# Kernel optimization log

Measured on AMD Instinct MI355X. Metric: run time of the kernel, lower is better.

Reference implementation:

```python
import jax, jax.numpy as jnp
import numpy as np
import math

D_MODEL, NHEAD, FACTOR = 512, 8, 5

def setup_inputs() -> dict:
    key = jax.random.key(0)
    ks = jax.random.split(key, 9)
    B, L = 4, 2048
    s = 0.02
    inp = {"x": jax.random.normal(ks[0], (B, L, D_MODEL), dtype=jnp.float32)}
    names = ["Wq", "bq", "Wk", "bk", "Wv", "bv", "Wo", "bo"]
    for i, n in enumerate(names):
        k = ks[i + 1]
        if n.startswith("W"):
            inp[n] = jax.random.normal(k, (D_MODEL, D_MODEL), dtype=jnp.float32) * s
        else:
            inp[n] = jnp.zeros((D_MODEL,), dtype=jnp.float32)
    return inp

def reference(x, Wq, bq, Wk, bk, Wv, bv, Wo, bo):
    B, L, _ = x.shape
    H = NHEAD
    D = D_MODEL // H
    # projections -> [B, H, L, D]
    def proj(W, b):
        return (x @ W + b).reshape(B, L, H, D).transpose(0, 2, 1, 3)
    Q, K, V = proj(Wq, bq), proj(Wk, bk), proj(Wv, bv)
    U = min(L, int(FACTOR * math.log(L)) if L > 1 else L)
    scores = jnp.einsum("bhqd,bhkd->bhqk", Q, K) / math.sqrt(D)
    # top-U threshold per query row, mask the rest to -inf
    topk_vals, _ = jax.lax.top_k(scores, U)          # [B,H,L,U]
    thr = topk_vals[..., -1:]                         # [B,H,L,1]
    scores = jnp.where(scores < thr, -jnp.inf, scores)
    attn = jax.nn.softmax(scores, axis=-1)           # dropout p=0 (eval)
    ctx = jnp.einsum("bhqk,bhkd->bhqd", attn, V)     # [B,H,L,D]
    ctx = ctx.transpose(0, 2, 1, 3).reshape(B, L, D_MODEL)
    return ctx @ Wo + bo
```

## Files before the change

### kernel.cpp

```cpp
#include <hip/hip_runtime.h>
#include <cstdint>
#include <cstddef>

#define D_MODEL 512
#define NHEAD   8
#define DH      64
#define B_SZ    4
#define L_SEQ   2048
#define U_TOP   38
#define QPB     8
#define KT      128

__device__ __forceinline__ unsigned mapmono(float f) {
    unsigned u = __float_as_uint(f);
    return (u & 0x80000000u) ? ~u : (u | 0x80000000u);
}

template<int MODE>
__global__ __launch_bounds__(256)
void gemm512(const float* __restrict__ A, const float* __restrict__ W,
             const float* __restrict__ bias, float* __restrict__ C)
{
    __shared__ float As[16][68];
    __shared__ float Bs[16][68];
    const int tid  = threadIdx.x;
    const int row0 = blockIdx.x * 64;
    const int col0 = blockIdx.y * 64;
    const int ty = tid >> 4, tx = tid & 15;
    float acc[4][4] = {};

    for (int kt = 0; kt < D_MODEL; kt += 16) {
        {
            const int m = tid >> 2, k = (tid & 3) << 2;
            const float4 a = *reinterpret_cast<const float4*>(
                &A[(size_t)(row0 + m) * D_MODEL + kt + k]);
            As[k + 0][m] = a.x; As[k + 1][m] = a.y;
            As[k + 2][m] = a.z; As[k + 3][m] = a.w;
        }
        {
            const int k = tid >> 4, n = (tid & 15) << 2;
            *reinterpret_cast<float4*>(&Bs[k][n]) =
                *reinterpret_cast<const float4*>(
                    &W[(size_t)(kt + k) * D_MODEL + col0 + n]);
        }
        __syncthreads();
        #pragma unroll
        for (int kk = 0; kk < 16; ++kk) {
            const float4 a4 = *reinterpret_cast<const float4*>(&As[kk][ty << 2]);
            const float4 b4 = *reinterpret_cast<const float4*>(&Bs[kk][tx << 2]);
            const float av[4] = {a4.x, a4.y, a4.z, a4.w};
            const float bv[4] = {b4.x, b4.y, b4.z, b4.w};
            #pragma unroll
            for (int i = 0; i < 4; ++i)
                #pragma unroll
                for (int j = 0; j < 4; ++j)
                    acc[i][j] += av[i] * bv[j];
        }
        __syncthreads();
    }

    #pragma unroll
    for (int i = 0; i < 4; ++i) {
        const int r = row0 + (ty << 2) + i;
        const int cb = col0 + (tx << 2);
        float4 v;
        v.x = acc[i][0] + bias[cb + 0];
        v.y = acc[i][1] + bias[cb + 1];
        v.z = acc[i][2] + bias[cb + 2];
        v.w = acc[i][3] + bias[cb + 3];
        if (MODE == 0) {
            *reinterpret_cast<float4*>(&C[(size_t)r * D_MODEL + cb]) = v;
        } else {
            const int b = r >> 11, l = r & (L_SEQ - 1);
            const int h = cb >> 6, d = cb & 63;
            *reinterpret_cast<float4*>(
                &C[(size_t)((b * NHEAD + h) * L_SEQ + l) * DH + d]) = v;
        }
    }
}

__global__ __launch_bounds__(256)
void chain_gemm_qk(const float* __restrict__ x, const float* __restrict__ W,
                   const float* __restrict__ bias, float* __restrict__ Out)
{
    const int tid  = threadIdx.x;
    const int col  = blockIdx.y * 256 + tid;
    const int row0 = blockIdx.x * 16;

    float acc[16];
    #pragma unroll
    for (int r = 0; r < 16; ++r) acc[r] = 0.f;

    for (int k = 0; k < D_MODEL; k += 4) {
        const float w0 = W[(size_t)(k + 0) * D_MODEL + col];
        const float w1 = W[(size_t)(k + 1) * D_MODEL + col];
        const float w2 = W[(size_t)(k + 2) * D_MODEL + col];
        const float w3 = W[(size_t)(k + 3) * D_MODEL + col];
        #pragma unroll
        for (int r = 0; r < 16; ++r) {
            const float4 xv = *reinterpret_cast<const float4*>(
                &x[(size_t)(row0 + r) * D_MODEL + k]);
            acc[r] = __fmaf_rn(xv.x, w0, acc[r]);
            acc[r] = __fmaf_rn(xv.y, w1, acc[r]);
            acc[r] = __fmaf_rn(xv.z, w2, acc[r]);
            acc[r] = __fmaf_rn(xv.w, w3, acc[r]);
        }
    }

    const float bc = bias[col];
    const int h = col >> 6, d = col & 63;
    #pragma unroll
    for (int r = 0; r < 16; ++r) {
        const int row = row0 + r;
        const int b = row >> 11, l = row & (L_SEQ - 1);
        Out[((size_t)((b * NHEAD + h) * L_SEQ + l)) * DH + d] =
            __fadd_rn(acc[r], bc);
    }
}

__global__ __launch_bounds__(512, 4)
void attn_kernel(const float* __restrict__ Q, const float* __restrict__ K,
                 const float* __restrict__ V, float* __restrict__ ctx)
{
    __shared__ float Qs[QPB][DH];
    __shared__ float Ks[KT * DH];
    __shared__ int   kidx[QPB][64];
    __shared__ float kwgt[QPB][64];

    const int bid = blockIdx.x;
    const int xcd = bid & 7, jrem = bid >> 3;
    const int bh  = xcd * 4 + (jrem >> 8);
    const int qt  = jrem & 255;
    const int b   = bh >> 3, h = bh & 7;

    const float* __restrict__ Qbh = Q + (size_t)bh * L_SEQ * DH;
    const float* __restrict__ Kbh = K + (size_t)bh * L_SEQ * DH;
    const float* __restrict__ Vbh = V + (size_t)bh * L_SEQ * DH;

    const int tid = threadIdx.x;
    const int wave = tid >> 6, lane = tid & 63;
    const int qg = wave;

    {
        const int q = tid >> 6, d = tid & 63;
        Qs[q][d] = Qbh[(size_t)(qt * QPB + q) * DH + d];
    }

    float s[32];

    #pragma unroll
    for (int t = 0; t < L_SEQ / KT; ++t) {
        __syncthreads();
        #pragma unroll
        for (int c = 0; c < 4; ++c) {
            const int f = c * 2048 + tid * 4;
            const int r = f >> 6, col = f & 63;
            const int sidx = (r << 6) + (col ^ ((r & 7) << 2));
            *reinterpret_cast<float4*>(&Ks[sidx]) =
                *reinterpret_cast<const float4*>(&Kbh[(size_t)t * (KT * DH) + f]);
        }
        __syncthreads();

        float v0 = 0.f, v1 = 0.f;
        #pragma unroll
        for (int dc = 0; dc < 16; ++dc) {
            const int sw = (dc ^ (lane & 7)) << 2;
            const float4 k0 = *reinterpret_cast<const float4*>(
                &Ks[(lane << 6) + sw]);
            const float4 k1 = *reinterpret_cast<const float4*>(
                &Ks[((64 + lane) << 6) + sw]);
            const float4 p = *reinterpret_cast<const float4*>(&Qs[qg][dc << 2]);
            v0 = __fmaf_rn(p.x, k0.x, v0);
            v0 = __fmaf_rn(p.y, k0.y, v0);
            v0 = __fmaf_rn(p.z, k0.z, v0);
            v0 = __fmaf_rn(p.w, k0.w, v0);
            v1 = __fmaf_rn(p.x, k1.x, v1);
            v1 = __fmaf_rn(p.y, k1.y, v1);
            v1 = __fmaf_rn(p.z, k1.z, v1);
            v1 = __fmaf_rn(p.w, k1.w, v1);
        }
        s[2*t]     = __fmul_rn(v0, 0.125f);
        s[2*t + 1] = __fmul_rn(v1, 0.125f);
    }

    #pragma unroll
    for (int j = 0; j < 32; ++j)
        s[j] = __uint_as_float(mapmono(s[j]));

    unsigned long long lo = 0ull, hi = 0x100000000ull;
    while (hi - lo > 1ull) {
        const unsigned mid = (unsigned)((lo + hi) >> 1);
        int cnt = 0;
        #pragma unroll
        for (int j = 0; j < 32; ++j)
            cnt += (int)__popcll(__ballot(__float_as_uint(s[j]) >= mid));
        if (cnt >= U_TOP) lo = mid; else hi = mid;
    }
    const unsigned thrU = (unsigned)lo;

    unsigned um = 0u;
    #pragma unroll
    for (int j = 0; j < 32; ++j) {
        const unsigned ub = __float_as_uint(s[j]);
        um = um > ub ? um : ub;
    }
    #pragma unroll
    for (int off = 32; off; off >>= 1) {
        const unsigned o = (unsigned)__shfl_xor((int)um, off);
        um = um > o ? um : o;
    }
    const float mrow = __uint_as_float((um & 0x80000000u) ? (um & 0x7FFFFFFFu) : ~um);

    int base = 0; float lsum = 0.f;
    #pragma unroll
    for (int j = 0; j < 32; ++j) {
        const unsigned ub = __float_as_uint(s[j]);
        const bool keep = (ub >= thrU);
        const unsigned long long mk = __ballot(keep);
        if (keep) {
            const float sc = __uint_as_float((ub & 0x80000000u) ? (ub & 0x7FFFFFFFu) : ~ub);
            const float w = __expf(sc - mrow);
            const int pos = base + (int)__popcll(mk & ((1ull << lane) - 1ull));
            if (pos < 64) {
                kidx[qg][pos] = ((j >> 1) << 7) + ((j & 1) << 6) + lane;
                kwgt[qg][pos] = w;
            }
            lsum += w;
        }
        base += (int)__popcll(mk);
    }
    #pragma unroll
    for (int off = 32; off; off >>= 1) lsum += __shfl_xor(lsum, off);
    const int nk = base < 64 ? base : 64;

    float acc = 0.f;
    int i = 0;
    for (; i + 8 <= nk; i += 8) {
        float wv[8], vv[8];
        #pragma unroll
        for (int u = 0; u < 8; ++u) {
            wv[u] = kwgt[qg][i + u];
            vv[u] = Vbh[(size_t)kidx[qg][i + u] * DH + lane];
        }
        #pragma unroll
        for (int u = 0; u < 8; ++u)
            acc = __fmaf_rn(wv[u], vv[u], acc);
    }
    for (; i < nk; ++i)
        acc = __fmaf_rn(kwgt[qg][i], Vbh[(size_t)kidx[qg][i] * DH + lane], acc);
    acc /= lsum;

    const int l = qt * QPB + qg;
    ctx[((size_t)(b * L_SEQ + l)) * D_MODEL + h * DH + lane] = acc;
}

extern "C" void kernel_launch(void* const* d_in, const int* in_sizes, int n_in,
                              void* d_out, int out_size, void* d_ws, size_t ws_size,
                              hipStream_t stream) {
    (void)in_sizes; (void)n_in; (void)out_size; (void)ws_size;
    const float* x  = (const float*)d_in[0];
    const float* Wq = (const float*)d_in[1];
    const float* bq = (const float*)d_in[2];
    const float* Wk = (const float*)d_in[3];
    const float* bk = (const float*)d_in[4];
    const float* Wv = (const float*)d_in[5];
    const float* bv = (const float*)d_in[6];
    const float* Wo = (const float*)d_in[7];
    const float* bo = (const float*)d_in[8];
    float* out = (float*)d_out;

    const size_t NE = (size_t)B_SZ * NHEAD * L_SEQ * DH;
    float* Qf = (float*)d_ws;
    float* Kf = Qf + NE;
    float* Vw = Kf + NE;
    float* Cw = Vw + NE;

    const dim3 gq(512, 2), g(128, 8), blk(256);
    chain_gemm_qk<<<gq, blk, 0, stream>>>(x, Wq, bq, Qf);
    chain_gemm_qk<<<gq, blk, 0, stream>>>(x, Wk, bk, Kf);
    gemm512<1>   <<<g,  blk, 0, stream>>>(x, Wv, bv, Vw);
    attn_kernel  <<<dim3(8192), dim3(512), 0, stream>>>(Qf, Kf, Vw, Cw);
    gemm512<0>   <<<g,  blk, 0, stream>>>(Cw, Wo, bo, out);
}
```

Before: 1.211 ms.

## Double-buffer K tiles in LDS with register prefetch in attention score loop

Replaces the load-sync-compute pattern for K tiles with a two-buffer LDS scheme. The next tile is prefetched into registers while the current tile is being consumed, which drops one barrier per iteration and overlaps global loads with the dot products. LDS use for K doubles, so the occupancy hint in launch bounds is lowered from 4 to 2 blocks per CU, which may reduce latency hiding elsewhere.

Result: slower. 1.704 ms (+40.7%).

```diff
diff --git a/kernel.cpp b/kernel.cpp
--- a/kernel.cpp
+++ b/kernel.cpp
@@ -10,6 +10,7 @@
 #define U_TOP   38
 #define QPB     8
 #define KT      128
+#define TILE_DW (KT * DH)
 
 __device__ __forceinline__ unsigned mapmono(float f) {
     unsigned u = __float_as_uint(f);
@@ -118,12 +119,12 @@
     }
 }
 
-__global__ __launch_bounds__(512, 4)
+__global__ __launch_bounds__(512, 2)
 void attn_kernel(const float* __restrict__ Q, const float* __restrict__ K,
                  const float* __restrict__ V, float* __restrict__ ctx)
 {
     __shared__ float Qs[QPB][DH];
-    __shared__ float Ks[KT * DH];
+    __shared__ float Ks[2 * TILE_DW];
     __shared__ int   kidx[QPB][64];
     __shared__ float kwgt[QPB][64];
 
@@ -142,33 +143,51 @@
     const int qg = wave;
 
     {
-        const int q = tid >> 6, d = tid & 63;
-        Qs[q][d] = Qbh[(size_t)(qt * QPB + q) * DH + d];
-    }
+        Qs[tid >> 6][tid & 63] =
+            Qbh[(size_t)(qt * QPB + (tid >> 6)) * DH + (tid & 63)];
+    }
+
+    const int fb = tid << 2;
+    int sidx[4];
+    #pragma unroll
+    for (int c = 0; c < 4; ++c) {
+        const int f = c * 2048 + fb;
+        const int r = f >> 6, col = f & 63;
+        sidx[c] = (r << 6) + (col ^ ((r & 7) << 2));
+    }
+
+    float4 stg0 = *reinterpret_cast<const float4*>(&Kbh[fb]);
+    float4 stg1 = *reinterpret_cast<const float4*>(&Kbh[2048 + fb]);
+    float4 stg2 = *reinterpret_cast<const float4*>(&Kbh[4096 + fb]);
+    float4 stg3 = *reinterpret_cast<const float4*>(&Kbh[6144 + fb]);
 
     float s[32];
 
     #pragma unroll
     for (int t = 0; t < L_SEQ / KT; ++t) {
+        float* buf = &Ks[(t & 1) * TILE_DW];
+        *reinterpret_cast<float4*>(&buf[sidx[0]]) = stg0;
+        *reinterpret_cast<float4*>(&buf[sidx[1]]) = stg1;
+        *reinterpret_cast<float4*>(&buf[sidx[2]]) = stg2;
+        *reinterpret_cast<float4*>(&buf[sidx[3]]) = stg3;
         __syncthreads();
-        #pragma unroll
-        for (int c = 0; c < 4; ++c) {
-            const int f = c * 2048 + tid * 4;
-            const int r = f >> 6, col = f & 63;
-            const int sidx = (r << 6) + (col ^ ((r & 7) << 2));
-            *reinterpret_cast<float4*>(&Ks[sidx]) =
-                *reinterpret_cast<const float4*>(&Kbh[(size_t)t * (KT * DH) + f]);
-        }
-        __syncthreads();
+
+        if (t < L_SEQ / KT - 1) {
+            const float* src = Kbh + (size_t)(t + 1) * TILE_DW;
+            stg0 = *reinterpret_cast<const float4*>(&src[fb]);
+            stg1 = *reinterpret_cast<const float4*>(&src[2048 + fb]);
+            stg2 = *reinterpret_cast<const float4*>(&src[4096 + fb]);
+            stg3 = *reinterpret_cast<const float4*>(&src[6144 + fb]);
+        }
 
         float v0 = 0.f, v1 = 0.f;
         #pragma unroll
         for (int dc = 0; dc < 16; ++dc) {
             const int sw = (dc ^ (lane & 7)) << 2;
             const float4 k0 = *reinterpret_cast<const float4*>(
-                &Ks[(lane << 6) + sw]);
+                &buf[(lane << 6) + sw]);
             const float4 k1 = *reinterpret_cast<const float4*>(
-                &Ks[((64 + lane) << 6) + sw]);
+                &buf[((64 + lane) << 6) + sw]);
             const float4 p = *reinterpret_cast<const float4*>(&Qs[qg][dc << 2]);
             v0 = __fmaf_rn(p.x, k0.x, v0);
             v0 = __fmaf_rn(p.y, k0.y, v0);
```

## Compute QK scores as 8x4 register tile per thread with LDS score slab

Applied to the files above, without the earlier changes.

Replaces the per-wave tiled QK^T loop, which staged K tiles through shared memory with repeated barriers, with a register-blocked scheme. Each thread reads K directly from global memory and accumulates scores for all 8 block queries across 4 keys, reusing each K load across queries. Mapped scores are written to a 64KB shared slab and reread per query wave for top-k selection. This removes LDS staging and most barriers, at the cost of lower occupancy, a large LDS footprint and uncoalesced strided global K reads.

New measurement: 1.944 ms. 60.5% more time.

```diff
diff --git a/kernel.cpp b/kernel.cpp
--- a/kernel.cpp
+++ b/kernel.cpp
@@ -9,7 +9,6 @@
 #define L_SEQ   2048
 #define U_TOP   38
 #define QPB     8
-#define KT      128
 
 __device__ __forceinline__ unsigned mapmono(float f) {
     unsigned u = __float_as_uint(f);
@@ -118,12 +117,12 @@
     }
 }
 
-__global__ __launch_bounds__(512, 4)
+__global__ __launch_bounds__(512, 2)
 void attn_kernel(const float* __restrict__ Q, const float* __restrict__ K,
                  const float* __restrict__ V, float* __restrict__ ctx)
 {
     __shared__ float Qs[QPB][DH];
-    __shared__ float Ks[KT * DH];
+    __shared__ float slab[QPB * L_SEQ];
     __shared__ int   kidx[QPB][64];
     __shared__ float kwgt[QPB][64];
 
@@ -139,53 +138,52 @@
 
     const int tid = threadIdx.x;
     const int wave = tid >> 6, lane = tid & 63;
+
+    Qs[tid >> 6][tid & 63] =
+        Qbh[(size_t)(qt * QPB + (tid >> 6)) * DH + (tid & 63)];
+    __syncthreads();
+
+    float acc[8][4];
+    #pragma unroll
+    for (int q = 0; q < 8; ++q)
+        #pragma unroll
+        for (int j = 0; j < 4; ++j) acc[q][j] = 0.f;
+
+    const int k0 = wave * 256 + lane;
+
+    #pragma unroll
+    for (int dc = 0; dc < 16; ++dc) {
+        float4 kv[4];
+        #pragma unroll
+        for (int j = 0; j < 4; ++j)
+            kv[j] = *reinterpret_cast<const float4*>(
+                &Kbh[(size_t)(k0 + j * 64) * DH + (dc << 2)]);
+        #pragma unroll
+        for (int q = 0; q < 8; ++q) {
+            const float4 p = *reinterpret_cast<const float4*>(&Qs[q][dc << 2]);
+            #pragma unroll
+            for (int j = 0; j < 4; ++j) {
+                acc[q][j] = __fmaf_rn(p.x, kv[j].x, acc[q][j]);
+                acc[q][j] = __fmaf_rn(p.y, kv[j].y, acc[q][j]);
+                acc[q][j] = __fmaf_rn(p.z, kv[j].z, acc[q][j]);
+                acc[q][j] = __fmaf_rn(p.w, kv[j].w, acc[q][j]);
+            }
+        }
+    }
+
+    #pragma unroll
+    for (int q = 0; q < 8; ++q)
+        #pragma unroll
+        for (int j = 0; j < 4; ++j)
+            slab[q * L_SEQ + wave * 256 + j * 64 + lane] =
+                __uint_as_float(mapmono(__fmul_rn(acc[q][j], 0.125f)));
+    __syncthreads();
+
     const int qg = wave;
-
-    {
-        const int q = tid >> 6, d = tid & 63;
-        Qs[q][d] = Qbh[(size_t)(qt * QPB + q) * DH + d];
-    }
-
     float s[32];
-
-    #pragma unroll
-    for (int t = 0; t < L_SEQ / KT; ++t) {
-        __syncthreads();
-        #pragma unroll
-        for (int c = 0; c < 4; ++c) {
-            const int f = c * 2048 + tid * 4;
-            const int r = f >> 6, col = f & 63;
-            const int sidx = (r << 6) + (col ^ ((r & 7) << 2));
-            *reinterpret_cast<float4*>(&Ks[sidx]) =
-                *reinterpret_cast<const float4*>(&Kbh[(size_t)t * (KT * DH) + f]);
-        }
-        __syncthreads();
-
-        float v0 = 0.f, v1 = 0.f;
-        #pragma unroll
-        for (int dc = 0; dc < 16; ++dc) {
-            const int sw = (dc ^ (lane & 7)) << 2;
-            const float4 k0 = *reinterpret_cast<const float4*>(
-                &Ks[(lane << 6) + sw]);
-            const float4 k1 = *reinterpret_cast<const float4*>(
-                &Ks[((64 + lane) << 6) + sw]);
-            const float4 p = *reinterpret_cast<const float4*>(&Qs[qg][dc << 2]);
-            v0 = __fmaf_rn(p.x, k0.x, v0);
-            v0 = __fmaf_rn(p.y, k0.y, v0);
-            v0 = __fmaf_rn(p.z, k0.z, v0);
-            v0 = __fmaf_rn(p.w, k0.w, v0);
-            v1 = __fmaf_rn(p.x, k1.x, v1);
-            v1 = __fmaf_rn(p.y, k1.y, v1);
-            v1 = __fmaf_rn(p.z, k1.z, v1);
-            v1 = __fmaf_rn(p.w, k1.w, v1);
-        }
-        s[2*t]     = __fmul_rn(v0, 0.125f);
-        s[2*t + 1] = __fmul_rn(v1, 0.125f);
-    }
-
     #pragma unroll
     for (int j = 0; j < 32; ++j)
-        s[j] = __uint_as_float(mapmono(s[j]));
+        s[j] = slab[qg * L_SEQ + j * 64 + lane];
 
     unsigned long long lo = 0ull, hi = 0x100000000ull;
     while (hi - lo > 1ull) {
@@ -222,7 +220,7 @@
             const float w = __expf(sc - mrow);
             const int pos = base + (int)__popcll(mk & ((1ull << lane) - 1ull));
             if (pos < 64) {
-                kidx[qg][pos] = ((j >> 1) << 7) + ((j & 1) << 6) + lane;
+                kidx[qg][pos] = (j << 6) + lane;
                 kwgt[qg][pos] = w;
             }
             lsum += w;
@@ -233,7 +231,7 @@
     for (int off = 32; off; off >>= 1) lsum += __shfl_xor(lsum, off);
     const int nk = base < 64 ? base : 64;
 
-    float acc = 0.f;
+    float acc2 = 0.f;
     int i = 0;
     for (; i + 8 <= nk; i += 8) {
         float wv[8], vv[8];
@@ -244,14 +242,14 @@
         }
         #pragma unroll
         for (int u = 0; u < 8; ++u)
-            acc = __fmaf_rn(wv[u], vv[u], acc);
+            acc2 = __fmaf_rn(wv[u], vv[u], acc2);
     }
     for (; i < nk; ++i)
-        acc = __fmaf_rn(kwgt[qg][i], Vbh[(size_t)kidx[qg][i] * DH + lane], acc);
-    acc /= lsum;
+        acc2 = __fmaf_rn(kwgt[qg][i], Vbh[(size_t)kidx[qg][i] * DH + lane], acc2);
+    acc2 /= lsum;
 
     const int l = qt * QPB + qg;
-    ctx[((size_t)(b * L_SEQ + l)) * D_MODEL + h * DH + lane] = acc;
+    ctx[((size_t)(b * L_SEQ + l)) * D_MODEL + h * DH + lane] = acc2;
 }
 
 extern "C" void kernel_launch(void* const* d_in, const int* in_sizes, int n_in,
```
